# Optimization experiments

Hardware: AMD Instinct MI355X
Metric: run time of the kernel (lower is better)

The kernel has to match this reference:

```python
import jax, jax.numpy as jnp
import numpy as np

N_EDGES, N_CH = 4, 2
N_NODES = 8192
IN_C, OUT_C = 64, 64


def setup_inputs() -> dict:
    key = jax.random.key(0)
    k1, k2, k3, k4, k5 = jax.random.split(key, 5)
    A = jax.random.uniform(k1, (N_EDGES, N_NODES, N_NODES), dtype=jnp.float32)
    X = jax.random.normal(k2, (N_NODES, IN_C), dtype=jnp.float32)
    weight = jax.random.normal(k3, (N_EDGES, N_CH), dtype=jnp.float32)
    # torch Linear: weight [out, in], bias [out]
    lin_w = jax.random.normal(k4, (OUT_C, IN_C), dtype=jnp.float32) / np.sqrt(IN_C)
    lin_b = jax.random.normal(k5, (OUT_C,), dtype=jnp.float32) * 0.01
    bias = jnp.zeros((OUT_C,), dtype=jnp.float32)
    return {"A": A, "X": X, "weight": weight, "lin_w": lin_w, "lin_b": lin_b, "bias": bias}


def reference(A, X, weight, lin_w, lin_b, bias):
    # softmax over edge dim (dim=0), then the double loop collapses to a
    # per-edge scale: A_agg = sum_i (sum_j fw[i,j]) * A[i]
    fw = jax.nn.softmax(weight, axis=0)          # [E, C]
    scale = fw.sum(axis=1)                        # [E]
    A_agg = jnp.einsum('e,enm->nm', scale, A)     # [N, N]
    H = A_agg @ X                                 # [N, in_c]
    H = H @ lin_w.T + lin_b + bias                # [N, out_c]
    return H
```

## Files before the change

kernel.cpp:

```cpp
#include <hip/hip_runtime.h>
#include <math.h>


#define NN 8192
#define CH 64
#define RB 16
#define KT 128
#define NT (NN / KT)
#define NBLK (NN / RB)

#define AGG_STRIDE_S 136
#define AGG_HALF (RB * AGG_STRIDE_S)
#define HT_STRIDE 68
#define XFRAGS_PER_TILE 1024

typedef __attribute__((ext_vector_type(8))) short bf16x8;
typedef __attribute__((ext_vector_type(4))) float f32x4;

__device__ __forceinline__ unsigned f2bfu(float f) {
  unsigned u = __float_as_uint(f);
  return (u + 0x7FFFu + ((u >> 16) & 1u)) >> 16;
}

__global__ __launch_bounds__(256)
void gtn_packX(const float* __restrict__ X, unsigned* __restrict__ ws) {
  const int F = blockIdx.x * 256 + threadIdx.x;
  const int t = F >> 10, rem = F & 1023;
  const int wv = rem >> 8, kt = (rem >> 6) & 3, lane = rem & 63;
  const int fm = lane & 15, fg = lane >> 4;
  const int c = wv * 16 + fm;
  const int bk = t * KT + kt * 32 + fg * 8;
  uint4 o;
  o.x = f2bfu(X[(size_t)(bk + 0) * CH + c]) | (f2bfu(X[(size_t)(bk + 1) * CH + c]) << 16);
  o.y = f2bfu(X[(size_t)(bk + 2) * CH + c]) | (f2bfu(X[(size_t)(bk + 3) * CH + c]) << 16);
  o.z = f2bfu(X[(size_t)(bk + 4) * CH + c]) | (f2bfu(X[(size_t)(bk + 5) * CH + c]) << 16);
  o.w = f2bfu(X[(size_t)(bk + 6) * CH + c]) | (f2bfu(X[(size_t)(bk + 7) * CH + c]) << 16);
  *(uint4*)&ws[(size_t)F * 4] = o;
}

template<bool PACKED>
__global__ __launch_bounds__(256, 3)
void gtn_fused(const float* __restrict__ A, const float* __restrict__ X,
               const uint4* __restrict__ Xp,
               const float* __restrict__ Wt, const float* __restrict__ lw,
               const float* __restrict__ lb, const float* __restrict__ bias,
               float* __restrict__ out) {
  __shared__ __align__(16) short aggS[2][AGG_HALF];
  __shared__ __align__(16) float hT[RB * HT_STRIDE];

  const int tid = threadIdx.x;
  const int n0  = blockIdx.x * RB;

  float sc0, sc1, sc2, sc3;
  {
    float a0 = Wt[0], a1 = Wt[2], a2 = Wt[4], a3 = Wt[6];
    float b0 = Wt[1], b1 = Wt[3], b2 = Wt[5], b3 = Wt[7];
    float ma = fmaxf(fmaxf(a0, a1), fmaxf(a2, a3));
    float mb = fmaxf(fmaxf(b0, b1), fmaxf(b2, b3));
    float ea0 = expf(a0 - ma), ea1 = expf(a1 - ma), ea2 = expf(a2 - ma), ea3 = expf(a3 - ma);
    float eb0 = expf(b0 - mb), eb1 = expf(b1 - mb), eb2 = expf(b2 - mb), eb3 = expf(b3 - mb);
    float ra = 1.f / (ea0 + ea1 + ea2 + ea3);
    float rb = 1.f / (eb0 + eb1 + eb2 + eb3);
    sc0 = ea0 * ra + eb0 * rb;  sc1 = ea1 * ra + eb1 * rb;
    sc2 = ea2 * ra + eb2 * rb;  sc3 = ea3 * ra + eb3 * rb;
  }

  const int rg = tid >> 4, cg = tid & 15;
  const int lane = tid & 63, wv = tid >> 6;
  const int ch0 = wv * 16;
  const int fm = lane & 15, fg = lane >> 4;

  const unsigned rowOff = (unsigned)((n0 + rg) * NN + cg * 4);

  auto loadA = [&](int t, float4* d) {
    const unsigned tOff = rowOff + (unsigned)(t * KT);
#pragma unroll
    for (int e = 0; e < 4; ++e) {
      const float* Ae = A + ((size_t)e << 26);
#pragma unroll
      for (int h = 0; h < 2; ++h)
        d[e * 2 + h] = *(const float4*)(Ae + tOff + h * 64);
    }
  };

  auto loadX = [&](int t, uint4* dst) {
    if constexpr (PACKED) {
      const uint4* xb = Xp + (size_t)t * XFRAGS_PER_TILE + wv * 256 + lane;
#pragma unroll
      for (int kt = 0; kt < 4; ++kt) dst[kt] = xb[kt * 64];
    } else {
#pragma unroll
      for (int kt = 0; kt < 4; ++kt) {
        const int bk = t * KT + kt * 32 + fg * 8;
        unsigned p[4];
#pragma unroll
        for (int pj = 0; pj < 4; ++pj)
          p[pj] = f2bfu(X[(size_t)(bk + 2 * pj) * CH + ch0 + fm]) |
                  (f2bfu(X[(size_t)(bk + 2 * pj + 1) * CH + ch0 + fm]) << 16);
        dst[kt] = make_uint4(p[0], p[1], p[2], p[3]);
      }
    }
  };

  auto combine = [&](const float4* a, int b) {
#pragma unroll
    for (int h = 0; h < 2; ++h) {
      float4 v0 = a[0 + h], v1 = a[2 + h], v2 = a[4 + h], v3 = a[6 + h];
      float gx = fmaf(sc3, v3.x, fmaf(sc2, v2.x, fmaf(sc1, v1.x, sc0 * v0.x)));
      float gy = fmaf(sc3, v3.y, fmaf(sc2, v2.y, fmaf(sc1, v1.y, sc0 * v0.y)));
      float gz = fmaf(sc3, v3.z, fmaf(sc2, v2.z, fmaf(sc1, v1.z, sc0 * v0.z)));
      float gw = fmaf(sc3, v3.w, fmaf(sc2, v2.w, fmaf(sc1, v1.w, sc0 * v0.w)));
      unsigned u0 = f2bfu(gx) | (f2bfu(gy) << 16);
      unsigned u1 = f2bfu(gz) | (f2bfu(gw) << 16);
      *(uint2*)&aggS[b][rg * AGG_STRIDE_S + h * 64 + cg * 4] = make_uint2(u0, u1);
    }
  };

  f32x4 acc = {0.f, 0.f, 0.f, 0.f};
  auto domfma = [&](int b, const uint4* xf) {
#pragma unroll
    for (int kt = 0; kt < 4; ++kt) {
      bf16x8 af = *(const bf16x8*)&aggS[b][fm * AGG_STRIDE_S + kt * 32 + fg * 8];
      union { uint4 q; bf16x8 v; } xu; xu.q = xf[kt];
      acc = __builtin_amdgcn_mfma_f32_16x16x32_bf16(af, xu.v, acc, 0, 0, 0);
    }
  };

  float4 aA[8], aB[8];
  uint4  xA[4], xB[4];
  loadA(0, aA); loadX(0, xA);

  for (int t = 0; t < NT; t += 2) {
    loadA(t + 1, aB); loadX(t + 1, xB);
    combine(aA, 0);
    asm volatile("s_waitcnt lgkmcnt(0)\n\ts_barrier" ::: "memory");
    domfma(0, xA);

    if (t + 2 < NT) { loadA(t + 2, aA); loadX(t + 2, xA); }
    combine(aB, 1);
    asm volatile("s_waitcnt lgkmcnt(0)\n\ts_barrier" ::: "memory");
    domfma(1, xB);
  }

  __syncthreads();
#pragma unroll
  for (int r = 0; r < 4; ++r)
    hT[(fg * 4 + r) * HT_STRIDE + ch0 + fm] = acc[r];
  __syncthreads();

  const int c0 = cg * 4;
  float s0 = lb[c0 + 0] + bias[c0 + 0];
  float s1 = lb[c0 + 1] + bias[c0 + 1];
  float s2 = lb[c0 + 2] + bias[c0 + 2];
  float s3 = lb[c0 + 3] + bias[c0 + 3];
#pragma unroll
  for (int k4 = 0; k4 < CH / 4; ++k4) {
    float4 hv = *(const float4*)&hT[rg * HT_STRIDE + k4 * 4];
    float4 w0 = *(const float4*)&lw[(size_t)(c0 + 0) * CH + k4 * 4];
    float4 w1 = *(const float4*)&lw[(size_t)(c0 + 1) * CH + k4 * 4];
    float4 w2 = *(const float4*)&lw[(size_t)(c0 + 2) * CH + k4 * 4];
    float4 w3 = *(const float4*)&lw[(size_t)(c0 + 3) * CH + k4 * 4];
    s0 += hv.x * w0.x + hv.y * w0.y + hv.z * w0.z + hv.w * w0.w;
    s1 += hv.x * w1.x + hv.y * w1.y + hv.z * w1.z + hv.w * w1.w;
    s2 += hv.x * w2.x + hv.y * w2.y + hv.z * w2.z + hv.w * w2.w;
    s3 += hv.x * w3.x + hv.y * w3.y + hv.z * w3.z + hv.w * w3.w;
  }
  *(float4*)&out[(size_t)(n0 + rg) * CH + c0] = make_float4(s0, s1, s2, s3);
}

extern "C" void kernel_launch(void* const* d_in, const int* in_sizes, int n_in,
                              void* d_out, int out_size, void* d_ws, size_t ws_size,
                              hipStream_t stream) {
  const float* A    = (const float*)d_in[0];
  const float* X    = (const float*)d_in[1];
  const float* Wt   = (const float*)d_in[2];
  const float* lw   = (const float*)d_in[3];
  const float* lb   = (const float*)d_in[4];
  const float* bias = (const float*)d_in[5];
  float* out = (float*)d_out;

  const size_t packBytes = (size_t)NT * XFRAGS_PER_TILE * 16;
  if (ws_size >= packBytes) {
    gtn_packX<<<dim3(256), 256, 0, stream>>>(X, (unsigned*)d_ws);
    gtn_fused<true><<<dim3(NBLK), 256, 0, stream>>>(
        A, X, (const uint4*)d_ws, Wt, lw, lb, bias, out);
  } else {
    gtn_fused<false><<<dim3(NBLK), 256, 0, stream>>>(
        A, X, nullptr, Wt, lw, lb, bias, out);
  }
}
```

Before: 192.8 us.

## Split K dimension across two blocks with partial-sum finalize kernel

Splits the K loop over two blocks per row tile, writing partial H results to workspace, and adds a finalize kernel that sums the partials and applies the linear layer. It also switches A loads to nontemporal, loads X fragments just-in-time rather than double-buffered to cut registers, and raises the occupancy hint from 3 to 4. The aim is more blocks in flight for this memory-bound 1 GB stream of A, at the cost of an extra launch and partial-buffer traffic. This only applies when the workspace is large enough.

```diff
diff --git a/kernel.cpp b/kernel.cpp
--- a/kernel.cpp
+++ b/kernel.cpp
@@ -13,6 +13,7 @@
 #define AGG_HALF (RB * AGG_STRIDE_S)
 #define HT_STRIDE 68
 #define XFRAGS_PER_TILE 1024
+#define WS_PARTIAL_OFF (4u << 20)
 
 typedef __attribute__((ext_vector_type(8))) short bf16x8;
 typedef __attribute__((ext_vector_type(4))) float f32x4;
@@ -38,18 +39,22 @@
   *(uint4*)&ws[(size_t)F * 4] = o;
 }
 
-template<bool PACKED>
-__global__ __launch_bounds__(256, 3)
+template<bool PACKED, int KSPLIT>
+__global__ __launch_bounds__(256, 4)
 void gtn_fused(const float* __restrict__ A, const float* __restrict__ X,
-               const uint4* __restrict__ Xp,
+               const uint4* __restrict__ Xp, float* __restrict__ partial,
                const float* __restrict__ Wt, const float* __restrict__ lw,
                const float* __restrict__ lb, const float* __restrict__ bias,
                float* __restrict__ out) {
+  constexpr int NT2 = NT / KSPLIT;
   __shared__ __align__(16) short aggS[2][AGG_HALF];
   __shared__ __align__(16) float hT[RB * HT_STRIDE];
 
   const int tid = threadIdx.x;
-  const int n0  = blockIdx.x * RB;
+  const int mt  = blockIdx.x % NBLK;
+  const int ks  = blockIdx.x / NBLK;
+  const int n0  = mt * RB;
+  const int tBase = ks * NT2;
 
   float sc0, sc1, sc2, sc3;
   {
@@ -72,26 +77,26 @@
 
   const unsigned rowOff = (unsigned)((n0 + rg) * NN + cg * 4);
 
-  auto loadA = [&](int t, float4* d) {
-    const unsigned tOff = rowOff + (unsigned)(t * KT);
+  auto loadA = [&](int t, f32x4* d) {
+    const unsigned tOff = rowOff + (unsigned)((tBase + t) * KT);
 #pragma unroll
     for (int e = 0; e < 4; ++e) {
       const float* Ae = A + ((size_t)e << 26);
 #pragma unroll
       for (int h = 0; h < 2; ++h)
-        d[e * 2 + h] = *(const float4*)(Ae + tOff + h * 64);
+        d[e * 2 + h] = __builtin_nontemporal_load((const f32x4*)(Ae + tOff + h * 64));
     }
   };
 
   auto loadX = [&](int t, uint4* dst) {
     if constexpr (PACKED) {
-      const uint4* xb = Xp + (size_t)t * XFRAGS_PER_TILE + wv * 256 + lane;
+      const uint4* xb = Xp + (size_t)(tBase + t) * XFRAGS_PER_TILE + wv * 256 + lane;
 #pragma unroll
       for (int kt = 0; kt < 4; ++kt) dst[kt] = xb[kt * 64];
     } else {
 #pragma unroll
       for (int kt = 0; kt < 4; ++kt) {
-        const int bk = t * KT + kt * 32 + fg * 8;
+        const int bk = (tBase + t) * KT + kt * 32 + fg * 8;
         unsigned p[4];
 #pragma unroll
         for (int pj = 0; pj < 4; ++pj)
@@ -102,10 +107,10 @@
     }
   };
 
-  auto combine = [&](const float4* a, int b) {
+  auto combine = [&](const f32x4* a, int b) {
 #pragma unroll
     for (int h = 0; h < 2; ++h) {
-      float4 v0 = a[0 + h], v1 = a[2 + h], v2 = a[4 + h], v3 = a[6 + h];
+      f32x4 v0 = a[0 + h], v1 = a[2 + h], v2 = a[4 + h], v3 = a[6 + h];
       float gx = fmaf(sc3, v3.x, fmaf(sc2, v2.x, fmaf(sc1, v1.x, sc0 * v0.x)));
       float gy = fmaf(sc3, v3.y, fmaf(sc2, v2.y, fmaf(sc1, v1.y, sc0 * v0.y)));
       float gz = fmaf(sc3, v3.z, fmaf(sc2, v2.z, fmaf(sc1, v1.z, sc0 * v0.z)));
@@ -126,26 +131,69 @@
     }
   };
 
-  float4 aA[8], aB[8];
-  uint4  xA[4], xB[4];
-  loadA(0, aA); loadX(0, xA);
-
-  for (int t = 0; t < NT; t += 2) {
-    loadA(t + 1, aB); loadX(t + 1, xB);
+  f32x4 aA[8], aB[8];
+  uint4 xC[4];
+  loadA(0, aA);
+
+  for (int t = 0; t < NT2; t += 2) {
+    loadA(t + 1, aB);
     combine(aA, 0);
     asm volatile("s_waitcnt lgkmcnt(0)\n\ts_barrier" ::: "memory");
-    domfma(0, xA);
-
-    if (t + 2 < NT) { loadA(t + 2, aA); loadX(t + 2, xA); }
+    loadX(t, xC);
+    domfma(0, xC);
+
+    if (t + 2 < NT2) loadA(t + 2, aA);
     combine(aB, 1);
     asm volatile("s_waitcnt lgkmcnt(0)\n\ts_barrier" ::: "memory");
-    domfma(1, xB);
-  }
-
-  __syncthreads();
-#pragma unroll
-  for (int r = 0; r < 4; ++r)
-    hT[(fg * 4 + r) * HT_STRIDE + ch0 + fm] = acc[r];
+    loadX(t + 1, xC);
+    domfma(1, xC);
+  }
+
+  if constexpr (KSPLIT == 2) {
+    float* P = partial + ((size_t)ks * NN + n0) * CH;
+#pragma unroll
+    for (int r = 0; r < 4; ++r)
+      P[(size_t)(fg * 4 + r) * CH + ch0 + fm] = acc[r];
+  } else {
+    __syncthreads();
+#pragma unroll
+    for (int r = 0; r < 4; ++r)
+      hT[(fg * 4 + r) * HT_STRIDE + ch0 + fm] = acc[r];
+    __syncthreads();
+
+    const int c0 = cg * 4;
+    float s0 = lb[c0 + 0] + bias[c0 + 0];
+    float s1 = lb[c0 + 1] + bias[c0 + 1];
+    float s2 = lb[c0 + 2] + bias[c0 + 2];
+    float s3 = lb[c0 + 3] + bias[c0 + 3];
+#pragma unroll
+    for (int k4 = 0; k4 < CH / 4; ++k4) {
+      float4 hv = *(const float4*)&hT[rg * HT_STRIDE + k4 * 4];
+      float4 w0 = *(const float4*)&lw[(size_t)(c0 + 0) * CH + k4 * 4];
+      float4 w1 = *(const float4*)&lw[(size_t)(c0 + 1) * CH + k4 * 4];
+      float4 w2 = *(const float4*)&lw[(size_t)(c0 + 2) * CH + k4 * 4];
+      float4 w3 = *(const float4*)&lw[(size_t)(c0 + 3) * CH + k4 * 4];
+      s0 += hv.x * w0.x + hv.y * w0.y + hv.z * w0.z + hv.w * w0.w;
+      s1 += hv.x * w1.x + hv.y * w1.y + hv.z * w1.z + hv.w * w1.w;
+      s2 += hv.x * w2.x + hv.y * w2.y + hv.z * w2.z + hv.w * w2.w;
+      s3 += hv.x * w3.x + hv.y * w3.y + hv.z * w3.z + hv.w * w3.w;
+    }
+    *(float4*)&out[(size_t)(n0 + rg) * CH + c0] = make_float4(s0, s1, s2, s3);
+  }
+}
+
+__global__ __launch_bounds__(256)
+void gtn_fin(const float* __restrict__ P, const float* __restrict__ lw,
+             const float* __restrict__ lb, const float* __restrict__ bias,
+             float* __restrict__ out) {
+  __shared__ __align__(16) float hT[RB * HT_STRIDE];
+  const int tid = threadIdx.x, rg = tid >> 4, cg = tid & 15;
+  const int n0 = blockIdx.x * RB;
+
+  float4 a = *(const float4*)&P[(size_t)(n0 + rg) * CH + cg * 4];
+  float4 b = *(const float4*)&P[(size_t)(NN + n0 + rg) * CH + cg * 4];
+  *(float4*)&hT[rg * HT_STRIDE + cg * 4] =
+      make_float4(a.x + b.x, a.y + b.y, a.z + b.z, a.w + b.w);
   __syncthreads();
 
   const int c0 = cg * 4;
@@ -179,13 +227,21 @@
   const float* bias = (const float*)d_in[5];
   float* out = (float*)d_out;
 
-  const size_t packBytes = (size_t)NT * XFRAGS_PER_TILE * 16;
-  if (ws_size >= packBytes) {
+  const size_t packBytes  = (size_t)NT * XFRAGS_PER_TILE * 16;
+  const size_t splitBytes = WS_PARTIAL_OFF + (size_t)2 * NN * CH * 4;
+
+  if (ws_size >= splitBytes) {
+    float* partial = (float*)((char*)d_ws + WS_PARTIAL_OFF);
     gtn_packX<<<dim3(256), 256, 0, stream>>>(X, (unsigned*)d_ws);
-    gtn_fused<true><<<dim3(NBLK), 256, 0, stream>>>(
-        A, X, (const uint4*)d_ws, Wt, lw, lb, bias, out);
+    gtn_fused<true, 2><<<dim3(NBLK * 2), 256, 0, stream>>>(
+        A, X, (const uint4*)d_ws, partial, Wt, lw, lb, bias, out);
+    gtn_fin<<<dim3(NBLK), 256, 0, stream>>>(partial, lw, lb, bias, out);
+  } else if (ws_size >= packBytes) {
+    gtn_packX<<<dim3(256), 256, 0, stream>>>(X, (unsigned*)d_ws);
+    gtn_fused<true, 1><<<dim3(NBLK), 256, 0, stream>>>(
+        A, X, (const uint4*)d_ws, nullptr, Wt, lw, lb, bias, out);
   } else {
-    gtn_fused<false><<<dim3(NBLK), 256, 0, stream>>>(
-        A, X, nullptr, Wt, lw, lb, bias, out);
-  }
-}
+    gtn_fused<false, 1><<<dim3(NBLK), 256, 0, stream>>>(
+        A, X, nullptr, nullptr, Wt, lw, lb, bias, out);
+  }
+}
```

New measurement: 192.0 us, median of 2. About the same (-0.4%).

## Drop X prepack kernel, use nontemporal A loads, load X just-in-time

Applied to the files above, without the earlier changes.

Removes the separate X bf16 packing kernel and workspace path, so every block reads and converts fp32 X from global memory itself. X is now loaded right before each MFMA stage rather than prefetched a tile ahead. A loads become nontemporal to avoid polluting cache with the streamed 1 GiB adjacency. Launch bounds drop from 3 to 2 blocks per CU, which allows more registers. Risks: X loads now sit on the critical path before the MFMAs, the strided fp32 reads add conversion work, and occupancy is lower.

```diff
diff --git a/kernel.cpp b/kernel.cpp
--- a/kernel.cpp
+++ b/kernel.cpp
@@ -12,7 +12,6 @@
 #define AGG_STRIDE_S 136
 #define AGG_HALF (RB * AGG_STRIDE_S)
 #define HT_STRIDE 68
-#define XFRAGS_PER_TILE 1024
 
 typedef __attribute__((ext_vector_type(8))) short bf16x8;
 typedef __attribute__((ext_vector_type(4))) float f32x4;
@@ -22,26 +21,8 @@
   return (u + 0x7FFFu + ((u >> 16) & 1u)) >> 16;
 }
 
-__global__ __launch_bounds__(256)
-void gtn_packX(const float* __restrict__ X, unsigned* __restrict__ ws) {
-  const int F = blockIdx.x * 256 + threadIdx.x;
-  const int t = F >> 10, rem = F & 1023;
-  const int wv = rem >> 8, kt = (rem >> 6) & 3, lane = rem & 63;
-  const int fm = lane & 15, fg = lane >> 4;
-  const int c = wv * 16 + fm;
-  const int bk = t * KT + kt * 32 + fg * 8;
-  uint4 o;
-  o.x = f2bfu(X[(size_t)(bk + 0) * CH + c]) | (f2bfu(X[(size_t)(bk + 1) * CH + c]) << 16);
-  o.y = f2bfu(X[(size_t)(bk + 2) * CH + c]) | (f2bfu(X[(size_t)(bk + 3) * CH + c]) << 16);
-  o.z = f2bfu(X[(size_t)(bk + 4) * CH + c]) | (f2bfu(X[(size_t)(bk + 5) * CH + c]) << 16);
-  o.w = f2bfu(X[(size_t)(bk + 6) * CH + c]) | (f2bfu(X[(size_t)(bk + 7) * CH + c]) << 16);
-  *(uint4*)&ws[(size_t)F * 4] = o;
-}
-
-template<bool PACKED>
-__global__ __launch_bounds__(256, 3)
+__global__ __launch_bounds__(256, 2)
 void gtn_fused(const float* __restrict__ A, const float* __restrict__ X,
-               const uint4* __restrict__ Xp,
                const float* __restrict__ Wt, const float* __restrict__ lw,
                const float* __restrict__ lb, const float* __restrict__ bias,
                float* __restrict__ out) {
@@ -72,40 +53,34 @@
 
   const unsigned rowOff = (unsigned)((n0 + rg) * NN + cg * 4);
 
-  auto loadA = [&](int t, float4* d) {
+  auto loadA = [&](int t, f32x4* d) {
     const unsigned tOff = rowOff + (unsigned)(t * KT);
 #pragma unroll
     for (int e = 0; e < 4; ++e) {
       const float* Ae = A + ((size_t)e << 26);
 #pragma unroll
       for (int h = 0; h < 2; ++h)
-        d[e * 2 + h] = *(const float4*)(Ae + tOff + h * 64);
+        d[e * 2 + h] = __builtin_nontemporal_load((const f32x4*)(Ae + tOff + h * 64));
     }
   };
 
   auto loadX = [&](int t, uint4* dst) {
-    if constexpr (PACKED) {
-      const uint4* xb = Xp + (size_t)t * XFRAGS_PER_TILE + wv * 256 + lane;
 #pragma unroll
-      for (int kt = 0; kt < 4; ++kt) dst[kt] = xb[kt * 64];
-    } else {
+    for (int kt = 0; kt < 4; ++kt) {
+      const int bk = t * KT + kt * 32 + fg * 8;
+      const float* xb = X + (size_t)bk * CH + ch0 + fm;
+      unsigned p[4];
 #pragma unroll
-      for (int kt = 0; kt < 4; ++kt) {
-        const int bk = t * KT + kt * 32 + fg * 8;
-        unsigned p[4];
-#pragma unroll
-        for (int pj = 0; pj < 4; ++pj)
-          p[pj] = f2bfu(X[(size_t)(bk + 2 * pj) * CH + ch0 + fm]) |
-                  (f2bfu(X[(size_t)(bk + 2 * pj + 1) * CH + ch0 + fm]) << 16);
-        dst[kt] = make_uint4(p[0], p[1], p[2], p[3]);
-      }
+      for (int pj = 0; pj < 4; ++pj)
+        p[pj] = f2bfu(xb[(2 * pj) * CH]) | (f2bfu(xb[(2 * pj + 1) * CH]) << 16);
+      dst[kt] = make_uint4(p[0], p[1], p[2], p[3]);
     }
   };
 
-  auto combine = [&](const float4* a, int b) {
+  auto combine = [&](const f32x4* a, int b) {
 #pragma unroll
     for (int h = 0; h < 2; ++h) {
-      float4 v0 = a[0 + h], v1 = a[2 + h], v2 = a[4 + h], v3 = a[6 + h];
+      f32x4 v0 = a[0 + h], v1 = a[2 + h], v2 = a[4 + h], v3 = a[6 + h];
       float gx = fmaf(sc3, v3.x, fmaf(sc2, v2.x, fmaf(sc1, v1.x, sc0 * v0.x)));
       float gy = fmaf(sc3, v3.y, fmaf(sc2, v2.y, fmaf(sc1, v1.y, sc0 * v0.y)));
       float gz = fmaf(sc3, v3.z, fmaf(sc2, v2.z, fmaf(sc1, v1.z, sc0 * v0.z)));
@@ -126,20 +101,22 @@
     }
   };
 
-  float4 aA[8], aB[8];
-  uint4  xA[4], xB[4];
-  loadA(0, aA); loadX(0, xA);
+  f32x4 aA[8], aB[8];
+  uint4 xC[4];
+  loadA(0, aA);
 
   for (int t = 0; t < NT; t += 2) {
-    loadA(t + 1, aB); loadX(t + 1, xB);
+    loadA(t + 1, aB);
     combine(aA, 0);
     asm volatile("s_waitcnt lgkmcnt(0)\n\ts_barrier" ::: "memory");
-    domfma(0, xA);
+    loadX(t, xC);
+    domfma(0, xC);
 
-    if (t + 2 < NT) { loadA(t + 2, aA); loadX(t + 2, xA); }
+    if (t + 2 < NT) loadA(t + 2, aA);
     combine(aB, 1);
     asm volatile("s_waitcnt lgkmcnt(0)\n\ts_barrier" ::: "memory");
-    domfma(1, xB);
+    loadX(t + 1, xC);
+    domfma(1, xC);
   }
 
   __syncthreads();
@@ -179,13 +156,5 @@
   const float* bias = (const float*)d_in[5];
   float* out = (float*)d_out;
 
-  const size_t packBytes = (size_t)NT * XFRAGS_PER_TILE * 16;
-  if (ws_size >= packBytes) {
-    gtn_packX<<<dim3(256), 256, 0, stream>>>(X, (unsigned*)d_ws);
-    gtn_fused<true><<<dim3(NBLK), 256, 0, stream>>>(
-        A, X, (const uint4*)d_ws, Wt, lw, lb, bias, out);
-  } else {
-    gtn_fused<false><<<dim3(NBLK), 256, 0, stream>>>(
-        A, X, nullptr, Wt, lw, lb, bias, out);
-  }
+  gtn_fused<<<dim3(NBLK), 256, 0, stream>>>(A, X, Wt, lw, lb, bias, out);
 }
```

Result: slower. 210.6 us (+9.3%).
